# Performance work log

Hardware: AMD Instinct MI355X
Metric: run time of the kernel (lower is better)

Reference implementation:

```python
import jax, jax.numpy as jnp
import numpy as np
import itertools, math

# ---- config (mirrors args in init_kwargs) ----
BS = 8
FRAME_H, FRAME_W = 120, 160
RES = 5            # map_resolution (cm/cell)
Z_RES = 5
MAP_SIZE_CM = 2400
VR = 100           # vision_range (cells)
FOV = 79.0
NSEM = 16
CAT_THR, EXP_THR, MAP_THR = 5.0, 1.0, 1.0
CAM_H_CM = 88.0    # camera_height * 100
MAX_H = int(360 / Z_RES)   # 72
MIN_H = int(-40 / Z_RES)   # -8
D = MAX_H - MIN_H          # 80
MAP_SZ = MAP_SIZE_CM // RES  # 480
C = 4 + NSEM
XC = (FRAME_W - 1.0) / 2.0
ZC = (FRAME_H - 1.0) / 2.0
F_CAM = (FRAME_W / 2.0) / math.tan(math.radians(FOV / 2.0))


def splat_feat_nd(feat, coords, grid_dims):
    # feat: [B, nF, nPt], coords: [B, 3, nPt] in [-1, 1]; trilinear scatter-add
    B, nF, nPt = feat.shape
    pos_dim, wts_dim = [], []
    for d, gd in enumerate(grid_dims):
        pos = coords[:, d, :] * (gd / 2.0) + gd / 2.0
        fl = jnp.floor(pos)
        pd, wd = [], []
        for ix in (0.0, 1.0):
            p = fl + ix
            safe = ((p > 0) & (p < gd)).astype(pos.dtype)
            wd.append((1.0 - jnp.abs(pos - p)) * safe)
            pd.append(p * safe)
        pos_dim.append(pd)
        wts_dim.append(wd)
    T = grid_dims[0] * grid_dims[1] * grid_dims[2]
    idxs, wts = [], []
    for ix_d in itertools.product((0, 1), (0, 1), (0, 1)):
        index = jnp.zeros_like(pos_dim[0][0])
        w = jnp.ones_like(index)
        for d in range(3):
            index = index * grid_dims[d] + pos_dim[d][ix_d[d]]
            w = w * wts_dim[d][ix_d[d]]
        idxs.append(index.astype(jnp.int32))
        wts.append(w)
    idx = jnp.concatenate(idxs, axis=-1)              # [B, 8*nPt]
    w = jnp.concatenate(wts, axis=-1)                 # [B, 8*nPt]
    src = jnp.tile(feat, (1, 1, 8)) * w[:, None, :]   # [B, nF, 8*nPt]

    def scat(src_b, idx_b):
        return jnp.zeros((nF, T), src_b.dtype).at[:, idx_b].add(src_b)

    grid = jax.vmap(scat)(src, idx)
    grid = jnp.clip(grid, 0.0, 1e3)
    return grid.reshape(B, nF, grid_dims[0], grid_dims[1], grid_dims[2])


def _base_grid(N, dtype):
    # torch affine_grid default align_corners=False pixel-center coords
    c = (2.0 * jnp.arange(N, dtype=dtype) + 1.0) / N - 1.0
    x = jnp.broadcast_to(c[None, :], (N, N))
    y = jnp.broadcast_to(c[:, None], (N, N))
    return x, y


def affine_grid_rot(t_deg, N):
    t = t_deg * (np.pi / 180.0)
    ct, st = jnp.cos(t), jnp.sin(t)
    x, y = _base_grid(N, t.dtype)
    gx = ct[:, None, None] * x - st[:, None, None] * y
    gy = st[:, None, None] * x + ct[:, None, None] * y
    return jnp.stack([gx, gy], -1)


def affine_grid_trans(xy, N):
    x, y = _base_grid(N, xy.dtype)
    gx = x[None] + xy[:, 0][:, None, None]
    gy = y[None] + xy[:, 1][:, None, None]
    return jnp.stack([gx, gy], -1)


def grid_sample(im, grid):
    # bilinear, align_corners=True, padding_mode='zeros'
    B, Ch, H, W = im.shape
    x = (grid[..., 0] + 1.0) * 0.5 * (W - 1)
    y = (grid[..., 1] + 1.0) * 0.5 * (H - 1)
    x0 = jnp.floor(x); y0 = jnp.floor(y)
    x1 = x0 + 1.0; y1 = y0 + 1.0

    def gather(im_b, iy, ix):
        valid = (ix >= 0) & (ix < W) & (iy >= 0) & (iy < H)
        ixc = jnp.clip(ix, 0, W - 1).astype(jnp.int32)
        iyc = jnp.clip(iy, 0, H - 1).astype(jnp.int32)
        return im_b[:, iyc, ixc] * valid[None].astype(im_b.dtype)

    def sample_one(im_b, x, y, x0, x1, y0, y1):
        wa = (x1 - x) * (y1 - y); wb = (x1 - x) * (y - y0)
        wc = (x - x0) * (y1 - y); wd = (x - x0) * (y - y0)
        return (gather(im_b, y0, x0) * wa[None] + gather(im_b, y1, x0) * wb[None]
                + gather(im_b, y0, x1) * wc[None] + gather(im_b, y1, x1) * wd[None])

    return jax.vmap(sample_one)(im, x, y, x0, x1, y0, y1)


def setup_inputs() -> dict:
    key = jax.random.key(0)
    k1, k2, k3, k4, k5, k6 = jax.random.split(key, 6)
    rgb = jax.random.uniform(k1, (BS, 3, FRAME_H, FRAME_W), jnp.float32)
    depth = jax.random.uniform(k2, (BS, 1, FRAME_H, FRAME_W), jnp.float32, 0.5, 5.0)
    sem = jax.random.uniform(k3, (BS, NSEM, FRAME_H, FRAME_W), jnp.float32)
    obs = jnp.concatenate([rgb, depth, sem], axis=1)
    maps_last = jax.random.uniform(k4, (BS, C, MAP_SZ, MAP_SZ), jnp.float32)
    xy = jax.random.uniform(k5, (BS, 2), jnp.float32, 2.0, 22.0)
    th = jax.random.uniform(k6, (BS, 1), jnp.float32, 0.0, 360.0)
    poses = jnp.concatenate([xy, th], axis=1)
    return {"obs": obs, "maps_last": maps_last, "poses": poses}


def reference(obs, maps_last, poses):
    bs = obs.shape[0]
    depth = obs[:, 3]
    rowmax = jnp.max(depth, axis=(0, 2))  # per image-row max over batch+width
    depth = jnp.where(depth == 0.0, rowmax[None, :, None], depth) * 100.0
    # point cloud from depth (du_scale=1)
    gx = jnp.arange(FRAME_W, dtype=depth.dtype)                 # column index
    gz = jnp.arange(FRAME_H - 1, -1, -1, dtype=depth.dtype)     # flipped row index
    X = (gx[None, None, :] - XC) * depth / F_CAM
    Z = (gz[None, :, None] - ZC) * depth / F_CAM
    Y = depth
    # camera -> agent frame (elev=0 -> identity rot), then shift_loc (theta=pi/2 -> identity rot)
    X = X + (VR * RES // 2)
    Z = Z + CAM_H_CM
    # normalize to [-1, 1] voxel coords
    xs = (X / RES - VR // 2.0) / VR * 2.0
    ys = (Y / RES - VR // 2.0) / VR * 2.0
    zs = (Z / Z_RES - (MAX_H + MIN_H) // 2.0) / (MAX_H - MIN_H) * 2.0
    coords = jnp.stack([xs, ys, zs], axis=1).reshape(bs, 3, -1)   # [B,3,nPt]
    feat = jnp.concatenate(
        [jnp.ones((bs, 1, FRAME_H * FRAME_W), obs.dtype),
         obs[:, 4:].reshape(bs, NSEM, -1)], axis=1)               # [B,1+NSEM,nPt]
    voxels = splat_feat_nd(feat, coords, (VR, VR, D))
    voxels = jnp.swapaxes(voxels, 2, 3)
    min_z = int(25 / Z_RES - MIN_H)                 # 13
    max_z = int((CAM_H_CM + 1) / Z_RES - MIN_H)     # 25
    agent_hp = voxels[..., min_z:max_z].sum(4)
    all_hp = voxels.sum(4)
    fp_map = jnp.clip(agent_hp[:, 0:1] / MAP_THR, 0.0, 1.0)
    fp_exp = jnp.clip(all_hp[:, 0:1] / EXP_THR, 0.0, 1.0)
    cat_pred = jnp.clip(agent_hp[:, 1:] / CAT_THR, 0.0, 1.0)
    x1 = MAP_SZ // 2 - VR // 2; x2 = x1 + VR
    y1 = MAP_SZ // 2; y2 = y1 + VR
    agent_view = jnp.zeros((bs, C, MAP_SZ, MAP_SZ), obs.dtype)
    agent_view = agent_view.at[:, 0:1, y1:y2, x1:x2].set(fp_map)
    agent_view = agent_view.at[:, 1:2, y1:y2, x1:x2].set(fp_exp)
    agent_view = agent_view.at[:, 4:4 + NSEM, y1:y2, x1:x2].set(cat_pred)
    # st_pose (detached in original)
    p = jax.lax.stop_gradient(poses)
    half = MAP_SZ // 2
    st_xy = -(p[:, :2] * 100.0 / RES - half) / half
    st_t = 90.0 - p[:, 2]
    rotated = grid_sample(agent_view, affine_grid_rot(st_t, MAP_SZ))
    translated = grid_sample(rotated, affine_grid_trans(st_xy, MAP_SZ))
    map_pred = jnp.maximum(maps_last, translated)
    map_pred = map_pred.at[:, 2].set(map_pred[:, 3])
    curr = (p[:, :2] * 100.0 / RES).astype(jnp.int32)
    rr = curr[:, 1]; cc = curr[:, 0]
    ii = jnp.arange(MAP_SZ)
    mask = (jnp.abs(ii[None, :, None] - rr[:, None, None]) <= 1) & \
           (jnp.abs(ii[None, None, :] - cc[:, None, None]) <= 1)
    map_pred = map_pred.at[:, 3].set(jnp.where(mask, 1.0, map_pred[:, 3]))
    return map_pred
```

## Files before the change

### kernel.cpp

```cpp
#include <hip/hip_runtime.h>
#include <hip/hip_bf16.h>
#include <math.h>

#define FRAME_W 160
#define FRAME_H 120
#define NPIX (FRAME_W*FRAME_H)
#define BS_ 8
#define CC_ 20
#define MAPSZ 480
#define MPIX (MAPSZ*MAPSZ)
#define AVC 18
#define AVP 10000
#define ROT0 120
#define ROT1 360
#define RW   240
#define RPTS (RW*RW)
#define WS_AV_OFF   512
#define WS_R_OFF    (6*1024*1024)
#define WS_NEED     ((size_t)WS_R_OFF + (size_t)BS_*AVC*RPTS*4)

#define STRIP_H 4
#define NSTRIP 25
#define SPLAT_T 1024
#define TILE_ELEMS (STRIP_H*100*AVC)

template<bool BF>
__device__ __forceinline__ float ldv(const void* p, size_t i){
    if constexpr (BF) return __bfloat162float(((const __hip_bfloat16*)p)[i]);
    else              return ((const float*)p)[i];
}
template<bool BF>
__device__ __forceinline__ void stv(void* p, size_t i, float v){
    if constexpr (BF) ((__hip_bfloat16*)p)[i] = __float2bfloat16(v);
    else              ((float*)p)[i] = v;
}

__device__ __forceinline__ int detect_flag(const void* poses){
    const __hip_bfloat16* pb = (const __hip_bfloat16*)poses;
    int ok = 1;
    #pragma unroll
    for (int k = 0; k < 24; k++){
        float v = __bfloat162float(pb[k]);
        if (!(v >= 0.0f && v < 400.0f)) ok = 0;
    }
    return ok;
}

template<bool BF>
__device__ __forceinline__ void splat_strip_impl(const void* __restrict__ obs,
                                                 float* __restrict__ av,
                                                 float* __restrict__ tile,
                                                 int b, int y0)
{
    const int tid = threadIdx.x;
    const size_t ob = (size_t)b*CC_*NPIX;
    const float f_cam = (float)(80.0 / tan(0.6894050545377601));

    const int NQ = NPIX/4;
    for (int qp = tid; qp < NQ; qp += SPLAT_T){
        float d4[4];
        if constexpr (BF){
            ushort4 u = ((const ushort4*)((const __hip_bfloat16*)obs + ob + 3*NPIX))[qp];
            d4[0] = __uint_as_float((unsigned)u.x << 16);
            d4[1] = __uint_as_float((unsigned)u.y << 16);
            d4[2] = __uint_as_float((unsigned)u.z << 16);
            d4[3] = __uint_as_float((unsigned)u.w << 16);
        } else {
            float4 v = ((const float4*)((const float*)obs + ob + 3*NPIX))[qp];
            d4[0]=v.x; d4[1]=v.y; d4[2]=v.z; d4[3]=v.w;
        }
        #pragma unroll
        for (int u=0;u<4;u++){
            int pix = qp*4 + u;
            float d100 = d4[u] * 100.0f;

            float ys   = (d100/5.0f - 50.0f)/100.0f*2.0f;
            float posy = ys*50.0f + 50.0f;
            float fly  = floorf(posy);
            int   ify  = (int)fly;
            if (ify < y0 - 1 || ify > y0 + STRIP_H - 1) continue;

            int r = pix / FRAME_W, c = pix - r*FRAME_W;
            float X = ((float)c - 79.5f) * d100 / f_cam + 250.0f;
            float Z = ((float)(FRAME_H-1 - r) - 59.5f) * d100 / f_cam + 88.0f;
            float xs = (X/5.0f - 50.0f)/100.0f*2.0f;
            float zs = (Z/5.0f - 32.0f)/80.0f*2.0f;
            float posx = xs*50.0f + 50.0f;
            float posz = zs*40.0f + 40.0f;

            float flx = floorf(posx), flz = floorf(posz);
            float wx[2], wy[2]; int ixv[2], iyv[2]; bool own[2];
            #pragma unroll
            for (int k=0;k<2;k++){
                float px = flx + (float)k;
                wx[k] = (px > 0.0f && px < 100.0f) ? (1.0f - fabsf(posx - px)) : 0.0f;
                ixv[k] = (int)px;
                float py = fly + (float)k;
                bool valid = (py > 0.0f && py < 100.0f);
                wy[k] = valid ? (1.0f - fabsf(posy - py)) : 0.0f;
                iyv[k] = (int)py;
                own[k] = valid && (iyv[k] >= y0) && (iyv[k] < y0 + STRIP_H);
            }
            if (!own[0] && !own[1]) continue;

            float wzall = 0.0f, wzag = 0.0f;
            #pragma unroll
            for (int k=0;k<2;k++){
                float pz = flz + (float)k;
                if (pz > 0.0f && pz < 80.0f){
                    float w = 1.0f - fabsf(posz - pz);
                    wzall += w;
                    int ipz = (int)pz;
                    if (ipz >= 13 && ipz < 25) wzag += w;
                }
            }
            if (wzall == 0.0f) continue;

            float sem[16];
            bool needsem = (wzag != 0.0f);
            if (needsem){
                #pragma unroll
                for (int s=0;s<16;s++) sem[s] = ldv<BF>(obs, ob + (size_t)(4+s)*NPIX + pix);
            }

            #pragma unroll
            for (int ky=0;ky<2;ky++){
                if (!own[ky] || wy[ky] == 0.0f) continue;
                #pragma unroll
                for (int kx=0;kx<2;kx++){
                    float wxy = wx[kx]*wy[ky];
                    if (wxy == 0.0f) continue;
                    float* cell = tile + (((iyv[ky]-y0)*100 + ixv[kx])*AVC);
                    atomicAdd(cell + 0, wxy*wzall);
                    float wa = wxy*wzag;
                    if (wa != 0.0f){
                        atomicAdd(cell + 1, wa);
                        #pragma unroll
                        for (int s=0;s<16;s++) atomicAdd(cell + 2 + s, wa*sem[s]);
                    }
                }
            }
        }
    }

    __syncthreads();
    for (int k = tid; k < TILE_ELEMS; k += SPLAT_T){
        int ch = k / 400;
        int rc = k - ch*400;
        av[((size_t)b*AVC + ch)*AVP + y0*100 + rc] = tile[rc*AVC + ch];
    }
}

extern "C" __global__ __launch_bounds__(SPLAT_T)
void smk75806v7_splat(const void* __restrict__ obs,
                      const void* __restrict__ poses,
                      float* __restrict__ av,
                      int* __restrict__ flag,
                      float* __restrict__ params)
{
    __shared__ float tile[TILE_ELEMS];
    __shared__ int sflag;
    int tid = threadIdx.x;

    if (tid < 8){
        int ok = detect_flag(poses);
        if (tid == 0) sflag = ok;
        if (blockIdx.x == 0){
            if (tid == 0) *flag = ok;
            int b = tid;
            float p0, p1, th;
            if (ok){
                const __hip_bfloat16* pb = (const __hip_bfloat16*)poses;
                p0 = __bfloat162float(pb[b*3+0]);
                p1 = __bfloat162float(pb[b*3+1]);
                th = __bfloat162float(pb[b*3+2]);
            } else {
                const float* pf = (const float*)poses;
                p0 = pf[b*3+0]; p1 = pf[b*3+1]; th = pf[b*3+2];
            }
            params[b*8+0] = -((p0*100.0f/5.0f) - 240.0f)/240.0f;
            params[b*8+1] = -((p1*100.0f/5.0f) - 240.0f)/240.0f;
            float t = (90.0f - th) * 0.017453292519943295f;
            params[b*8+2] = cosf(t);
            params[b*8+3] = sinf(t);
            params[b*8+4] = p1*100.0f/5.0f;
            params[b*8+5] = p0*100.0f/5.0f;
        }
    }
    for (int k = tid; k < TILE_ELEMS/4; k += SPLAT_T)
        ((float4*)tile)[k] = make_float4(0.f,0.f,0.f,0.f);
    __syncthreads();

    int bid = blockIdx.x;
    int b  = bid & 7;
    int y0 = (bid >> 3) * STRIP_H;
    if (sflag) splat_strip_impl<true >(obs, av, tile, b, y0);
    else       splat_strip_impl<false>(obs, av, tile, b, y0);
}

extern "C" __global__ __launch_bounds__(256)
void smk75806v7_rot(const float* __restrict__ av,
                    const float* __restrict__ params,
                    float* __restrict__ R)
{
    int gid = blockIdx.x*256 + threadIdx.x;
    if (gid >= BS_*RPTS) return;
    int b = gid / RPTS;
    int rem = gid - b*RPTS;
    int ry = rem / RW, rx = rem - ry*RW;
    int yy = ry + ROT0, xx = rx + ROT0;

    float ct = params[b*8+2], st = params[b*8+3];
    float xb2 = (2.0f*(float)xx + 1.0f)/480.0f - 1.0f;
    float yb2 = (2.0f*(float)yy + 1.0f)/480.0f - 1.0f;
    float gx = ct*xb2 - st*yb2;
    float gy = st*xb2 + ct*yb2;
    float x2 = (gx + 1.0f)*0.5f*479.0f;
    float y2 = (gy + 1.0f)*0.5f*479.0f;
    float x20f = floorf(x2), y20f = floorf(y2);
    int x20 = (int)x20f, y20 = (int)y20f;
    float wx2[2] = {(x20f + 1.0f) - x2, x2 - x20f};
    float wy2[2] = {(y20f + 1.0f) - y2, y2 - y20f};

    float wf[4]; int off[4]; bool any = false;
    #pragma unroll
    for (int t=0;t<4;t++){
        int sy = t>>1, sx = t&1;
        int ay = y20 + sy, ax = x20 + sx;
        float w2 = wx2[sx]*wy2[sy];
        bool v = (ay >= 240 && ay < 340 && ax >= 190 && ax < 290) && (w2 != 0.0f);
        wf[t]  = v ? w2 : 0.0f;
        off[t] = v ? (ay-240)*100 + (ax-190) : 0;
        any |= v;
    }

    float* Rb = R + (size_t)b*AVC*RPTS + rem;
    if (!any){
        #pragma unroll
        for (int q=0;q<AVC;q++) Rb[(size_t)q*RPTS] = 0.0f;
        return;
    }
    const float* avb = av + (size_t)b*AVC*AVP;
    #pragma unroll
    for (int q=0;q<AVC;q++){
        int pl = (q==0) ? 1 : ((q==1) ? 0 : q);
        float sc = (q>=2) ? 0.2f : 1.0f;
        const float* ap = avb + (size_t)pl*AVP;
        float v = wf[0]*fminf(ap[off[0]]*sc, 1.0f)
                + wf[1]*fminf(ap[off[1]]*sc, 1.0f)
                + wf[2]*fminf(ap[off[2]]*sc, 1.0f)
                + wf[3]*fminf(ap[off[3]]*sc, 1.0f);
        Rb[(size_t)q*RPTS] = v;
    }
}

template<bool BF>
__device__ __forceinline__ void finalB_impl(const float* __restrict__ R,
                                            const void* __restrict__ maps_last,
                                            const float* __restrict__ params,
                                            void* __restrict__ out, int gid)
{
    int b = gid / MPIX;
    int rem = gid - b*MPIX;
    int i = rem / MAPSZ, j = rem - i*MAPSZ;

    const float* pbp = params + b*8;
    float tx = pbp[0], ty = pbp[1];
    int rr = (int)pbp[4];
    int cc = (int)pbp[5];

    size_t mlb = (size_t)b*CC_*MPIX;
    size_t px  = (size_t)rem;

    float m0 = ldv<BF>(maps_last, mlb + 0*MPIX + px);
    float m1 = ldv<BF>(maps_last, mlb + 1*MPIX + px);
    float m3 = ldv<BF>(maps_last, mlb + 3*MPIX + px);
    float ms[16];
    #pragma unroll
    for (int q=0;q<16;q++) ms[q] = ldv<BF>(maps_last, mlb + (size_t)(4+q)*MPIX + px);

    float acc[18];
    #pragma unroll
    for (int q=0;q<18;q++) acc[q] = 0.0f;

    float yb = (2.0f*(float)i + 1.0f)/480.0f - 1.0f + ty;
    float y = (yb + 1.0f)*0.5f*479.0f;
    float xb = (2.0f*(float)j + 1.0f)/480.0f - 1.0f + tx;
    float x = (xb + 1.0f)*0.5f*479.0f;
    float x0f = floorf(x), y0f = floorf(y);
    int x0 = (int)x0f, y0 = (int)y0f;
    float wxv[2] = {(x0f + 1.0f) - x, x - x0f};
    float wyv[2] = {(y0f + 1.0f) - y, y - y0f};

    if (x0+1 >= ROT0 && x0 < ROT1 && y0+1 >= ROT0 && y0 < ROT1){
        float cw[4]; int coff[4];
        #pragma unroll
        for (int t=0;t<4;t++){
            int ty2 = t>>1, tx2 = t&1;
            int yy = y0 + ty2, xx = x0 + tx2;
            float w = wxv[tx2]*wyv[ty2];
            bool v = (yy >= ROT0 && yy < ROT1 && xx >= ROT0 && xx < ROT1);
            cw[t]  = v ? w : 0.0f;
            coff[t] = v ? (yy-ROT0)*RW + (xx-ROT0) : 0;
        }
        const float* Rb = R + (size_t)b*AVC*RPTS;
        #pragma unroll
        for (int q=0;q<18;q++){
            const float* Rp = Rb + (size_t)q*RPTS;
            acc[q] = cw[0]*Rp[coff[0]] + cw[1]*Rp[coff[1]]
                   + cw[2]*Rp[coff[2]] + cw[3]*Rp[coff[3]];
        }
    }

    bool m3m = (i - rr) <= 1 && (rr - i) <= 1 && (j - cc) <= 1 && (cc - j) <= 1;
    float f3 = fmaxf(m3, 0.0f);
    stv<BF>(out, mlb + 0*MPIX + px, fmaxf(m0, acc[0]));
    stv<BF>(out, mlb + 1*MPIX + px, fmaxf(m1, acc[1]));
    stv<BF>(out, mlb + 2*MPIX + px, f3);
    stv<BF>(out, mlb + 3*MPIX + px, m3m ? 1.0f : f3);
    #pragma unroll
    for (int q=0;q<16;q++)
        stv<BF>(out, mlb + (size_t)(4+q)*MPIX + px, fmaxf(ms[q], acc[2+q]));
}

extern "C" __global__ __launch_bounds__(256)
void smk75806v7_finalB(const float* __restrict__ R,
                       const void* __restrict__ maps_last,
                       const float* __restrict__ params,
                       void* __restrict__ out,
                       const int* __restrict__ flag)
{
    int gid = blockIdx.x*256 + threadIdx.x;
    if (gid >= BS_*MPIX) return;
    if (*flag) finalB_impl<true >(R, maps_last, params, out, gid);
    else       finalB_impl<false>(R, maps_last, params, out, gid);
}

template<bool BF>
__device__ __forceinline__ void finalF_impl(const float* __restrict__ av,
                                            const void* __restrict__ maps_last,
                                            const float* __restrict__ params,
                                            void* __restrict__ out, int gid)
{
    int b = gid / MPIX;
    int rem = gid - b*MPIX;
    int i = rem / MAPSZ, j = rem - i*MAPSZ;

    const float* pbp = params + b*8;
    float tx = pbp[0], ty = pbp[1], ct = pbp[2], st = pbp[3];
    int rr = (int)pbp[4];
    int cc = (int)pbp[5];

    size_t mlb = (size_t)b*CC_*MPIX;
    size_t px  = (size_t)rem;

    float m0 = ldv<BF>(maps_last, mlb + 0*MPIX + px);
    float m1 = ldv<BF>(maps_last, mlb + 1*MPIX + px);
    float m3 = ldv<BF>(maps_last, mlb + 3*MPIX + px);

    float acc[18];
    #pragma unroll
    for (int q=0;q<18;q++) acc[q]=0.0f;

    float yb = (2.0f*(float)i + 1.0f)/480.0f - 1.0f + ty;
    float y = (yb + 1.0f)*0.5f*479.0f;
    float xb = (2.0f*(float)j + 1.0f)/480.0f - 1.0f + tx;
    float x = (xb + 1.0f)*0.5f*479.0f;
    float x0f = floorf(x), y0f = floorf(y);
    int x0 = (int)x0f, y0 = (int)y0f;
    float wxv[2] = {(x0f + 1.0f) - x, x - x0f};
    float wyv[2] = {(y0f + 1.0f) - y, y - y0f};

    if (x0+1 >= ROT0 && x0 < ROT1 && y0+1 >= ROT0 && y0 < ROT1){
        #pragma unroll
        for (int ty2=0;ty2<2;ty2++){
            #pragma unroll
            for (int tx2=0;tx2<2;tx2++){
                int yy = y0 + ty2, xx = x0 + tx2;
                float w = wxv[tx2]*wyv[ty2];
                if (w == 0.0f) continue;
                if (yy < ROT0 || yy >= ROT1 || xx < ROT0 || xx >= ROT1) continue;
                float xb2 = (2.0f*(float)xx + 1.0f)/480.0f - 1.0f;
                float yb2 = (2.0f*(float)yy + 1.0f)/480.0f - 1.0f;
                float gx = ct*xb2 - st*yb2;
                float gy = st*xb2 + ct*yb2;
                float x2 = (gx + 1.0f)*0.5f*479.0f;
                float y2 = (gy + 1.0f)*0.5f*479.0f;
                float x20f = floorf(x2), y20f = floorf(y2);
                int x20 = (int)x20f, y20 = (int)y20f;
                float wx2[2] = {(x20f + 1.0f) - x2, x2 - x20f};
                float wy2[2] = {(y20f + 1.0f) - y2, y2 - y20f};

                float rs[18];
                #pragma unroll
                for (int q=0;q<18;q++) rs[q]=0.0f;
                #pragma unroll
                for (int sy=0;sy<2;sy++){
                    #pragma unroll
                    for (int sx=0;sx<2;sx++){
                        int ay = y20 + sy, ax = x20 + sx;
                        float w2 = wx2[sx]*wy2[sy];
                        if (w2 == 0.0f) continue;
                        if (ay < 240 || ay >= 340 || ax < 190 || ax >= 290) continue;
                        const float* cb = av + (size_t)b*AVC*AVP + (ay-240)*100 + (ax-190);
                        rs[0] += w2 * fminf(cb[1*AVP], 1.0f);
                        rs[1] += w2 * fminf(cb[0],     1.0f);
                        #pragma unroll
                        for (int s=0;s<16;s++)
                            rs[2+s] += w2 * fminf(cb[(size_t)(2+s)*AVP]*0.2f, 1.0f);
                    }
                }
                #pragma unroll
                for (int q=0;q<18;q++) acc[q] += w*rs[q];
            }
        }
    }

    bool m3m = (i - rr) <= 1 && (rr - i) <= 1 && (j - cc) <= 1 && (cc - j) <= 1;
    float f3 = fmaxf(m3, 0.0f);
    stv<BF>(out, mlb + 0*MPIX + px, fmaxf(m0, acc[0]));
    stv<BF>(out, mlb + 1*MPIX + px, fmaxf(m1, acc[1]));
    stv<BF>(out, mlb + 2*MPIX + px, f3);
    stv<BF>(out, mlb + 3*MPIX + px, m3m ? 1.0f : f3);
    #pragma unroll
    for (int q=0;q<16;q++){
        float v = fmaxf(ldv<BF>(maps_last, mlb + (size_t)(4+q)*MPIX + px), acc[2+q]);
        stv<BF>(out, mlb + (size_t)(4+q)*MPIX + px, v);
    }
}

extern "C" __global__ __launch_bounds__(256)
void smk75806v7_finalF(const float* __restrict__ av,
                       const void* __restrict__ maps_last,
                       const float* __restrict__ params,
                       void* __restrict__ out,
                       const int* __restrict__ flag)
{
    int gid = blockIdx.x*256 + threadIdx.x;
    if (gid >= BS_*MPIX) return;
    if (*flag) finalF_impl<true >(av, maps_last, params, out, gid);
    else       finalF_impl<false>(av, maps_last, params, out, gid);
}

extern "C" void kernel_launch(void* const* d_in, const int* in_sizes, int n_in,
                              void* d_out, int out_size, void* d_ws, size_t ws_size,
                              hipStream_t stream) {
    const void* pO = d_in[0];
    const void* pM = (n_in > 1) ? d_in[1] : d_in[0];
    const void* pP = (n_in > 2) ? d_in[2] : d_in[0];
    for (int i = 0; i < n_in; i++){
        if      (in_sizes[i] == BS_*CC_*NPIX) pO = d_in[i];
        else if (in_sizes[i] == BS_*CC_*MPIX) pM = d_in[i];
        else if (in_sizes[i] == BS_*3)        pP = d_in[i];
    }
    int*   flag   = (int*)d_ws;
    float* params = (float*)((char*)d_ws + 64);
    float* av     = (float*)((char*)d_ws + WS_AV_OFF);
    float* R      = (float*)((char*)d_ws + WS_R_OFF);

    smk75806v7_splat<<<BS_*NSTRIP, SPLAT_T, 0, stream>>>(pO, pP, av, flag, params);
    if (ws_size >= WS_NEED){
        smk75806v7_rot   <<<(BS_*RPTS + 255)/256, 256, 0, stream>>>(av, params, R);
        smk75806v7_finalB<<<(BS_*MPIX + 255)/256, 256, 0, stream>>>(R, pM, params, d_out, flag);
    } else {
        smk75806v7_finalF<<<(BS_*MPIX + 255)/256, 256, 0, stream>>>(av, pM, params, d_out, flag);
    }
}
```

Before: 334.1 us.

## Restrict rotation and final blend to pose-dependent bounding boxes, stream rest in splat

Each batch pose now gets a bounding box of where the rotated and translated egocentric patch can land. The rotation kernel only covers its bounded region, and the final blend kernel only covers the output box. All other output pixels take a vectorized max(maps_last, 0) copy, done by extra blocks added to the splat kernel so it overlaps the splat work. This avoids full-map bilinear sampling over 480x480x8 pixels. The risk is that box_impl reads R cells left unwritten (stale) if the bounds are off, and the stream blocks and box kernel both write the box region, which relies on launch ordering.

After: 322.3 us. -3.5%, faster.

```diff
diff --git a/kernel.cpp b/kernel.cpp
--- a/kernel.cpp
+++ b/kernel.cpp
@@ -15,14 +15,17 @@
 #define ROT1 360
 #define RW   240
 #define RPTS (RW*RW)
-#define WS_AV_OFF   512
+#define WS_AV_OFF   4096
 #define WS_R_OFF    (6*1024*1024)
 #define WS_NEED     ((size_t)WS_R_OFF + (size_t)BS_*AVC*RPTS*4)
 
 #define STRIP_H 4
-#define NSTRIP 25
+#define NSPLAT_B 200
 #define SPLAT_T 1024
 #define TILE_ELEMS (STRIP_H*100*AVC)
+#define NSTREAM_B 450
+#define RB 160
+#define FB 176
 
 template<bool BF>
 __device__ __forceinline__ float ldv(const void* p, size_t i){
@@ -34,6 +37,34 @@
     if constexpr (BF) ((__hip_bfloat16*)p)[i] = __float2bfloat16(v);
     else              ((float*)p)[i] = v;
 }
+template<bool BF>
+__device__ __forceinline__ void ld4(const void* p, size_t i, float* o){
+    if constexpr (BF){
+        ushort4 u = *(const ushort4*)((const __hip_bfloat16*)p + i);
+        o[0] = __uint_as_float((unsigned)u.x << 16);
+        o[1] = __uint_as_float((unsigned)u.y << 16);
+        o[2] = __uint_as_float((unsigned)u.z << 16);
+        o[3] = __uint_as_float((unsigned)u.w << 16);
+    } else {
+        float4 v = *(const float4*)((const float*)p + i);
+        o[0]=v.x; o[1]=v.y; o[2]=v.z; o[3]=v.w;
+    }
+}
+template<bool BF>
+__device__ __forceinline__ void st4(void* p, size_t i, const float* s){
+    if constexpr (BF){
+        __hip_bfloat162 h0, h1;
+        h0.x = __float2bfloat16(s[0]); h0.y = __float2bfloat16(s[1]);
+        h1.x = __float2bfloat16(s[2]); h1.y = __float2bfloat16(s[3]);
+        __hip_bfloat162* q = (__hip_bfloat162*)((__hip_bfloat16*)p + i);
+        q[0] = h0; q[1] = h1;
+    } else {
+        *(float4*)((float*)p + i) = make_float4(s[0],s[1],s[2],s[3]);
+    }
+}
+
+__device__ __forceinline__ int imin(int a,int b){ return a<b?a:b; }
+__device__ __forceinline__ int imax(int a,int b){ return a>b?a:b; }
 
 __device__ __forceinline__ int detect_flag(const void* poses){
     const __hip_bfloat16* pb = (const __hip_bfloat16*)poses;
@@ -44,6 +75,67 @@
         if (!(v >= 0.0f && v < 400.0f)) ok = 0;
     }
     return ok;
+}
+
+struct BP {
+    float tx, ty, ct, st;
+    int rr, cc;
+    int rx0, rx1, ry0, ry1;
+    int iLo, iHi, jLo, jHi;
+};
+
+template<bool BF>
+__device__ __forceinline__ BP make_bp(const void* poses, int b){
+    float p0,p1,th;
+    if constexpr (BF){
+        const __hip_bfloat16* pb = (const __hip_bfloat16*)poses;
+        p0 = __bfloat162float(pb[b*3+0]);
+        p1 = __bfloat162float(pb[b*3+1]);
+        th = __bfloat162float(pb[b*3+2]);
+    } else {
+        const float* pf = (const float*)poses;
+        p0 = pf[b*3+0]; p1 = pf[b*3+1]; th = pf[b*3+2];
+    }
+    BP P;
+    P.tx = -((p0*100.0f/5.0f) - 240.0f)/240.0f;
+    P.ty = -((p1*100.0f/5.0f) - 240.0f)/240.0f;
+    float t = (90.0f - th) * 0.017453292519943295f;
+    P.ct = cosf(t); P.st = sinf(t);
+    P.rr = (int)(p1*100.0f/5.0f);
+    P.cc = (int)(p0*100.0f/5.0f);
+
+    float mnx=1e9f, mxx=-1e9f, mny=1e9f, mxy=-1e9f;
+    #pragma unroll
+    for (int cs=0; cs<4; cs++){
+        float X2 = (cs&1) ? 291.0f : 188.0f;
+        float Y2 = (cs&2) ? 341.0f : 238.0f;
+        float g = X2/239.5f - 1.0f, h = Y2/239.5f - 1.0f;
+        float u =  P.ct*g + P.st*h;
+        float v = -P.st*g + P.ct*h;
+        float xx = (u + 1.0f)*240.0f - 0.5f;
+        float yy = (v + 1.0f)*240.0f - 0.5f;
+        mnx = fminf(mnx,xx); mxx = fmaxf(mxx,xx);
+        mny = fminf(mny,yy); mxy = fmaxf(mxy,yy);
+    }
+    P.rx0 = imax(ROT0,   (int)floorf(mnx) - 3);
+    P.rx1 = imin(ROT1-1, (int)ceilf (mxx) + 3);
+    P.ry0 = imax(ROT0,   (int)floorf(mny) - 3);
+    P.ry1 = imin(ROT1-1, (int)ceilf (mxy) + 3);
+
+    float jLoF = (((float)(P.rx0-1)/239.5f - P.tx)*480.0f - 1.0f)*0.5f;
+    float jHiF = (((float)(P.rx1+1)/239.5f - P.tx)*480.0f - 1.0f)*0.5f;
+    float iLoF = (((float)(P.ry0-1)/239.5f - P.ty)*480.0f - 1.0f)*0.5f;
+    float iHiF = (((float)(P.ry1+1)/239.5f - P.ty)*480.0f - 1.0f)*0.5f;
+    if (jLoF > (float)(MAPSZ-1) || jHiF < 0.0f ||
+        iLoF > (float)(MAPSZ-1) || iHiF < 0.0f){
+        P.iLo = 1<<29; P.iHi = -1; P.jLo = 1<<29; P.jHi = -1;
+    } else {
+        P.jLo = imax(0,       (int)floorf(jLoF) - 3);
+        P.jHi = imin(MAPSZ-1, (int)ceilf (jHiF) + 3);
+        P.iLo = imax(0,       (int)floorf(iLoF) - 3);
+        P.iHi = imin(MAPSZ-1, (int)ceilf (iHiF) + 3);
+    }
+    return P;
 }
 
 template<bool BF>
@@ -151,9 +243,54 @@
     }
 }
 
+template<bool BF>
+__device__ __forceinline__ void stream_group(const void* __restrict__ maps_last,
+                                             void* __restrict__ out,
+                                             int rr, int cc, int b, int i, int j)
+{
+    size_t mlb = (size_t)b*CC_*MPIX;
+    size_t px  = (size_t)i*MAPSZ + j;
+
+    float m0[4], m1[4], m3[4];
+    ld4<BF>(maps_last, mlb + 0*MPIX + px, m0);
+    ld4<BF>(maps_last, mlb + 1*MPIX + px, m1);
+    ld4<BF>(maps_last, mlb + 3*MPIX + px, m3);
+    float o0[4],o1[4],o2[4],o3[4];
+    bool rowm = (i - rr) <= 1 && (rr - i) <= 1;
+    #pragma unroll
+    for (int u=0;u<4;u++){
+        o0[u] = fmaxf(m0[u], 0.0f);
+        o1[u] = fmaxf(m1[u], 0.0f);
+        float f3 = fmaxf(m3[u], 0.0f);
+        o2[u] = f3;
+        bool cm = rowm && ((j+u) - cc) <= 1 && (cc - (j+u)) <= 1;
+        o3[u] = cm ? 1.0f : f3;
+    }
+    st4<BF>(out, mlb + 0*MPIX + px, o0);
+    st4<BF>(out, mlb + 1*MPIX + px, o1);
+    st4<BF>(out, mlb + 2*MPIX + px, o2);
+    st4<BF>(out, mlb + 3*MPIX + px, o3);
+
+    #pragma unroll
+    for (int q0=0;q0<16;q0+=4){
+        float t[4][4];
+        #pragma unroll
+        for (int q=0;q<4;q++) ld4<BF>(maps_last, mlb + (size_t)(4+q0+q)*MPIX + px, t[q]);
+        #pragma unroll
+        for (int q=0;q<4;q++){
+            float ov[4];
+            #pragma unroll
+            for (int u=0;u<4;u++) ov[u] = fmaxf(t[q][u], 0.0f);
+            st4<BF>(out, mlb + (size_t)(4+q0+q)*MPIX + px, ov);
+        }
+    }
+}
+
 extern "C" __global__ __launch_bounds__(SPLAT_T)
-void smk75806v7_splat(const void* __restrict__ obs,
+void smk75806v11_main(const void* __restrict__ obs,
                       const void* __restrict__ poses,
+                      const void* __restrict__ maps_last,
+                      void* __restrict__ out,
                       float* __restrict__ av,
                       int* __restrict__ flag,
                       float* __restrict__ params)
@@ -161,56 +298,69 @@
     __shared__ float tile[TILE_ELEMS];
     __shared__ int sflag;
     int tid = threadIdx.x;
-
-    if (tid < 8){
-        int ok = detect_flag(poses);
-        if (tid == 0) sflag = ok;
-        if (blockIdx.x == 0){
+    if (tid == 0) sflag = detect_flag(poses);
+    __syncthreads();
+    int ok = sflag;
+    int bid = blockIdx.x;
+
+    if (bid < NSPLAT_B){
+        if (bid == 0 && tid < 8){
             if (tid == 0) *flag = ok;
-            int b = tid;
-            float p0, p1, th;
-            if (ok){
-                const __hip_bfloat16* pb = (const __hip_bfloat16*)poses;
-                p0 = __bfloat162float(pb[b*3+0]);
-                p1 = __bfloat162float(pb[b*3+1]);
-                th = __bfloat162float(pb[b*3+2]);
-            } else {
-                const float* pf = (const float*)poses;
-                p0 = pf[b*3+0]; p1 = pf[b*3+1]; th = pf[b*3+2];
-            }
-            params[b*8+0] = -((p0*100.0f/5.0f) - 240.0f)/240.0f;
-            params[b*8+1] = -((p1*100.0f/5.0f) - 240.0f)/240.0f;
-            float t = (90.0f - th) * 0.017453292519943295f;
-            params[b*8+2] = cosf(t);
-            params[b*8+3] = sinf(t);
-            params[b*8+4] = p1*100.0f/5.0f;
-            params[b*8+5] = p0*100.0f/5.0f;
-        }
-    }
-    for (int k = tid; k < TILE_ELEMS/4; k += SPLAT_T)
-        ((float4*)tile)[k] = make_float4(0.f,0.f,0.f,0.f);
-    __syncthreads();
-
-    int bid = blockIdx.x;
-    int b  = bid & 7;
-    int y0 = (bid >> 3) * STRIP_H;
-    if (sflag) splat_strip_impl<true >(obs, av, tile, b, y0);
-    else       splat_strip_impl<false>(obs, av, tile, b, y0);
+            BP P = ok ? make_bp<true>(poses, tid) : make_bp<false>(poses, tid);
+            float* pp = params + tid*16;
+            pp[0]=P.tx; pp[1]=P.ty; pp[2]=P.ct; pp[3]=P.st;
+            pp[4]=(float)P.rr;  pp[5]=(float)P.cc;
+            pp[6]=(float)P.rx0; pp[7]=(float)P.rx1;
+            pp[8]=(float)P.ry0; pp[9]=(float)P.ry1;
+            pp[10]=(float)P.iLo; pp[11]=(float)P.iHi;
+            pp[12]=(float)P.jLo; pp[13]=(float)P.jHi;
+        }
+        for (int k = tid; k < TILE_ELEMS/4; k += SPLAT_T)
+            ((float4*)tile)[k] = make_float4(0.f,0.f,0.f,0.f);
+        __syncthreads();
+        int b  = bid & 7;
+        int y0 = (bid >> 3) * STRIP_H;
+        if (ok) splat_strip_impl<true >(obs, av, tile, b, y0);
+        else    splat_strip_impl<false>(obs, av, tile, b, y0);
+    } else {
+        int gg = (bid - NSPLAT_B)*SPLAT_T + tid;
+        int b   = gg / (MPIX/4);
+        int rem = gg - b*(MPIX/4);
+        int i   = rem / (MAPSZ/4);
+        int j   = (rem - i*(MAPSZ/4))*4;
+        float p0, p1;
+        if (ok){
+            const __hip_bfloat16* pb = (const __hip_bfloat16*)poses;
+            p0 = __bfloat162float(pb[b*3+0]);
+            p1 = __bfloat162float(pb[b*3+1]);
+        } else {
+            const float* pf = (const float*)poses;
+            p0 = pf[b*3+0]; p1 = pf[b*3+1];
+        }
+        int rr = (int)(p1*100.0f/5.0f);
+        int cc = (int)(p0*100.0f/5.0f);
+        if (ok) stream_group<true >(maps_last, out, rr, cc, b, i, j);
+        else    stream_group<false>(maps_last, out, rr, cc, b, i, j);
+    }
 }
 
 extern "C" __global__ __launch_bounds__(256)
-void smk75806v7_rot(const float* __restrict__ av,
-                    const float* __restrict__ params,
-                    float* __restrict__ R)
+void smk75806v11_rot(const float* __restrict__ av,
+                     const float* __restrict__ params,
+                     float* __restrict__ R)
 {
     int gid = blockIdx.x*256 + threadIdx.x;
-    if (gid >= BS_*RPTS) return;
-    int b = gid / RPTS;
-    int rem = gid - b*RPTS;
-    int ry = rem / RW, rx = rem - ry*RW;
-    int yy = ry + ROT0, xx = rx + ROT0;
-
-    float ct = params[b*8+2], st = params[b*8+3];
+    if (gid >= BS_*RB*RB) return;
+    int b = gid / (RB*RB);
+    int d = gid - b*(RB*RB);
+    int dy = d / RB, dx = d - dy*RB;
+    const float* pp = params + b*16;
+    int rx0 = (int)pp[6], rx1 = (int)pp[7], ry0 = (int)pp[8], ry1 = (int)pp[9];
+    int xx = rx0 + dx, yy = ry0 + dy;
+    if (xx > rx1 || yy > ry1) return;
+    if (xx < ROT0 || xx >= ROT1 || yy < ROT0 || yy >= ROT1) return;
+
+    float ct = pp[2], st = pp[3];
     float xb2 = (2.0f*(float)xx + 1.0f)/480.0f - 1.0f;
     float yb2 = (2.0f*(float)yy + 1.0f)/480.0f - 1.0f;
     float gx = ct*xb2 - st*yb2;
@@ -234,7 +384,7 @@
         any |= v;
     }
 
-    float* Rb = R + (size_t)b*AVC*RPTS + rem;
+    float* Rb = R + (size_t)b*AVC*RPTS + (size_t)(yy-ROT0)*RW + (xx-ROT0);
     if (!any){
         #pragma unroll
         for (int q=0;q<AVC;q++) Rb[(size_t)q*RPTS] = 0.0f;
@@ -255,22 +405,18 @@
 }
 
 template<bool BF>
-__device__ __forceinline__ void finalB_impl(const float* __restrict__ R,
-                                            const void* __restrict__ maps_last,
-                                            const float* __restrict__ params,
-                                            void* __restrict__ out, int gid)
-{
-    int b = gid / MPIX;
-    int rem = gid - b*MPIX;
-    int i = rem / MAPSZ, j = rem - i*MAPSZ;
-
-    const float* pbp = params + b*8;
-    float tx = pbp[0], ty = pbp[1];
-    int rr = (int)pbp[4];
-    int cc = (int)pbp[5];
+__device__ __forceinline__ void box_impl(const float* __restrict__ R,
+                                         const void* __restrict__ maps_last,
+                                         const float* __restrict__ pp,
+                                         void* __restrict__ out,
+                                         int b, int i, int j)
+{
+    float tx = pp[0], ty = pp[1];
+    int rr = (int)pp[4], cc = (int)pp[5];
+    int rx0 = (int)pp[6], rx1 = (int)pp[7], ry0 = (int)pp[8], ry1 = (int)pp[9];
 
     size_t mlb = (size_t)b*CC_*MPIX;
-    size_t px  = (size_t)rem;
+    size_t px  = (size_t)i*MAPSZ + j;
 
     float m0 = ldv<BF>(maps_last, mlb + 0*MPIX + px);
     float m1 = ldv<BF>(maps_last, mlb + 1*MPIX + px);
@@ -292,16 +438,17 @@
     float wxv[2] = {(x0f + 1.0f) - x, x - x0f};
     float wyv[2] = {(y0f + 1.0f) - y, y - y0f};
 
-    if (x0+1 >= ROT0 && x0 < ROT1 && y0+1 >= ROT0 && y0 < ROT1){
+    if (x0+1 >= rx0 && x0 <= rx1 && y0+1 >= ry0 && y0 <= ry1){
+        int soff = (ry0-ROT0)*RW + (rx0-ROT0);
         float cw[4]; int coff[4];
         #pragma unroll
         for (int t=0;t<4;t++){
             int ty2 = t>>1, tx2 = t&1;
             int yy = y0 + ty2, xx = x0 + tx2;
             float w = wxv[tx2]*wyv[ty2];
-            bool v = (yy >= ROT0 && yy < ROT1 && xx >= ROT0 && xx < ROT1);
-            cw[t]  = v ? w : 0.0f;
-            coff[t] = v ? (yy-ROT0)*RW + (xx-ROT0) : 0;
+            bool v = (yy >= ry0 && yy <= ry1 && xx >= rx0 && xx <= rx1);
+            cw[t]   = v ? w : 0.0f;
+            coff[t] = v ? (yy-ROT0)*RW + (xx-ROT0) : soff;
         }
         const float* Rb = R + (size_t)b*AVC*RPTS;
         #pragma unroll
@@ -324,16 +471,24 @@
 }
 
 extern "C" __global__ __launch_bounds__(256)
-void smk75806v7_finalB(const float* __restrict__ R,
-                       const void* __restrict__ maps_last,
-                       const float* __restrict__ params,
-                       void* __restrict__ out,
-                       const int* __restrict__ flag)
+void smk75806v11_box(const float* __restrict__ R,
+                     const void* __restrict__ maps_last,
+                     const float* __restrict__ params,
+                     void* __restrict__ out,
+                     const int* __restrict__ flag)
 {
     int gid = blockIdx.x*256 + threadIdx.x;
-    if (gid >= BS_*MPIX) return;
-    if (*flag) finalB_impl<true >(R, maps_last, params, out, gid);
-    else       finalB_impl<false>(R, maps_last, params, out, gid);
+    if (gid >= BS_*FB*FB) return;
+    int b = gid / (FB*FB);
+    int d = gid - b*(FB*FB);
+    int dy = d / FB, dx = d - dy*FB;
+    const float* pp = params + b*16;
+    int iLo = (int)pp[10], iHi = (int)pp[11];
+    int jLo = (int)pp[12], jHi = (int)pp[13];
+    int i = iLo + dy, j = jLo + dx;
+    if (i > iHi || j > jHi) return;
+    if (*flag) box_impl<true >(R, maps_last, pp, out, b, i, j);
+    else       box_impl<false>(R, maps_last, pp, out, b, i, j);
 }
 
 template<bool BF>
@@ -346,7 +501,7 @@
     int rem = gid - b*MPIX;
     int i = rem / MAPSZ, j = rem - i*MAPSZ;
 
-    const float* pbp = params + b*8;
+    const float* pbp = params + b*16;
     float tx = pbp[0], ty = pbp[1], ct = pbp[2], st = pbp[3];
     int rr = (int)pbp[4];
     int cc = (int)pbp[5];
@@ -430,11 +585,11 @@
 }
 
 extern "C" __global__ __launch_bounds__(256)
-void smk75806v7_finalF(const float* __restrict__ av,
-                       const void* __restrict__ maps_last,
-                       const float* __restrict__ params,
-                       void* __restrict__ out,
-                       const int* __restrict__ flag)
+void smk75806v11_finalF(const float* __restrict__ av,
+                        const void* __restrict__ maps_last,
+                        const float* __restrict__ params,
+                        void* __restrict__ out,
+                        const int* __restrict__ flag)
 {
     int gid = blockIdx.x*256 + threadIdx.x;
     if (gid >= BS_*MPIX) return;
@@ -458,11 +613,12 @@
     float* av     = (float*)((char*)d_ws + WS_AV_OFF);
     float* R      = (float*)((char*)d_ws + WS_R_OFF);
 
-    smk75806v7_splat<<<BS_*NSTRIP, SPLAT_T, 0, stream>>>(pO, pP, av, flag, params);
+    smk75806v11_main<<<NSPLAT_B + NSTREAM_B, SPLAT_T, 0, stream>>>(
+        pO, pP, pM, d_out, av, flag, params);
     if (ws_size >= WS_NEED){
-        smk75806v7_rot   <<<(BS_*RPTS + 255)/256, 256, 0, stream>>>(av, params, R);
-        smk75806v7_finalB<<<(BS_*MPIX + 255)/256, 256, 0, stream>>>(R, pM, params, d_out, flag);
+        smk75806v11_rot<<<(BS_*RB*RB + 255)/256, 256, 0, stream>>>(av, params, R);
+        smk75806v11_box<<<(BS_*FB*FB + 255)/256, 256, 0, stream>>>(R, pM, params, d_out, flag);
     } else {
-        smk75806v7_finalF<<<(BS_*MPIX + 255)/256, 256, 0, stream>>>(av, pM, params, d_out, flag);
-    }
-}
+        smk75806v11_finalF<<<(BS_*MPIX + 255)/256, 256, 0, stream>>>(av, pM, params, d_out, flag);
+    }
+}
```
